# Performance work log

Hardware: AMD Instinct MI355X
Metric: run time of the kernel (lower is better)

The kernel has to match this reference:

```python
import jax, jax.numpy as jnp
import numpy as np

K_SIGN = 100000.0   # tanh sharpness approximating sign()
EPS = 1e-05         # acos clamp epsilon


def setup_inputs() -> dict:
    key = jax.random.key(0)
    B, N, KV = 2, 8, 64
    contour = jax.random.uniform(key, (B, N, KV, 2), dtype=jnp.float32)  # values in [0,1]
    return {"contour": contour, "size": 128}


def reference(contour, size):
    b, n, kv, _ = contour.shape
    dt = contour.dtype
    # pixel grid, normalized by size (matches torch meshgrid 'ij' + reshape(-1,2)/size)
    g = jnp.arange(size, dtype=dt)
    mesh = jnp.stack(jnp.meshgrid(g, g, indexing="ij"), axis=-1).reshape(-1, 2) / size  # (S2, 2)

    c = contour.reshape(b * n, 1, kv, 2)          # (bn, 1, kv, 2)
    diff = c - mesh[None, :, None, :]             # (bn, S2, kv, 2)
    roll_diff = jnp.roll(diff, -1, axis=2)        # next vertex

    # sign = diff * swap(roll_diff); sign[...,1]-sign[...,0] = d_y*rd_x - d_x*rd_y
    cross = diff[..., 1] * roll_diff[..., 0] - diff[..., 0] * roll_diff[..., 1]
    sign = jnp.tanh(K_SIGN * cross)               # (bn, S2, kv)

    norm_diff = jnp.linalg.norm(diff, axis=3)
    norm_roll = jnp.linalg.norm(roll_diff, axis=3)
    scalar = jnp.sum(diff * roll_diff, axis=3)
    cosang = jnp.clip(scalar / (norm_diff * norm_roll), -1.0 + EPS, 1.0 - EPS)
    angles = jnp.arccos(cosang)                   # (bn, S2, kv)

    sum_angles = jnp.clip(jnp.abs(jnp.sum(sign * angles, axis=2) / (2.0 * jnp.pi)), 0.0, 1.0)
    return sum_angles.reshape(b, n, size, size)
```

## Files before the change

### kernel.cpp

```cpp
#include <hip/hip_runtime.h>
#include <math.h>

#define BLOCK 256
#define MAX_KV_LDS 1024


__device__ __forceinline__ float fast_tanh(float t)
{
    float e = __expf(2.0f * t);
    return 1.0f - 2.0f * __builtin_amdgcn_rcpf(e + 1.0f);
}

__device__ __forceinline__ float fast_acos(float x)
{
    float y = fabsf(x);
    float p = -0.0187293f;
    p = fmaf(p, y, 0.0742610f);
    p = fmaf(p, y, -0.2121144f);
    p = fmaf(p, y, 1.5707288f);
    float a = sqrtf(1.0f - y) * p;
    return (x >= 0.0f) ? a : (3.14159265358979f - a);
}

template <typename VP>
__device__ __forceinline__ float winding_sum(VP vsrc, int kv, float mx, float my)
{
    float acc = 0.0f;
    float2 v0 = vsrc[0];
    float dx = v0.x - mx;
    float dy = v0.y - my;
    const float d0x = dx, d0y = dy;
    float nd2 = fmaf(dx, dx, dy * dy);
    const float nd02 = nd2;

    #pragma unroll 4
    for (int k = 0; k < kv - 1; ++k) {
        float2 vn = vsrc[k + 1];
        float rx = vn.x - mx;
        float ry = vn.y - my;
        float cross = dy * rx - dx * ry;
        float dot   = fmaf(dx, rx, dy * ry);
        float nr2   = fmaf(rx, rx, ry * ry);
        float cosang = dot * __builtin_amdgcn_rsqf(nd2 * nr2);
        cosang = fminf(fmaxf(cosang, -1.0f + 1e-5f), 1.0f - 1e-5f);
        acc = fmaf(fast_tanh(100000.0f * cross), fast_acos(cosang), acc);
        dx = rx; dy = ry; nd2 = nr2;
    }
    {
        float cross = dy * d0x - dx * d0y;
        float dot   = fmaf(dx, d0x, dy * d0y);
        float cosang = dot * __builtin_amdgcn_rsqf(nd2 * nd02);
        cosang = fminf(fmaxf(cosang, -1.0f + 1e-5f), 1.0f - 1e-5f);
        acc = fmaf(fast_tanh(100000.0f * cross), fast_acos(cosang), acc);
    }
    return acc;
}

__global__ __launch_bounds__(BLOCK)
void contour_mask_kernel(const float2* __restrict__ contour,
                         const int* __restrict__ size_ptr,
                         float* __restrict__ out,
                         int out_size, int in0_elems)
{
    __shared__ float2 verts[MAX_KV_LDS];

    const int size     = *size_ptr;
    const int S2       = size * size;
    const int bn_total = out_size / S2;
    const int kv       = in0_elems / (bn_total * 2);

    const int idx     = blockIdx.x * BLOCK + threadIdx.x;
    const int bn0     = (blockIdx.x * BLOCK) / S2;
    const int bn_last = (blockIdx.x * BLOCK + BLOCK - 1) / S2;
    const bool use_lds = (kv <= MAX_KV_LDS) && (bn0 == bn_last);

    if (use_lds) {
        for (int i = threadIdx.x; i < kv; i += BLOCK)
            verts[i] = contour[(size_t)bn0 * kv + i];
    }
    __syncthreads();

    if (idx >= out_size) return;

    const int bn = idx / S2;
    const int p  = idx - bn * S2;
    const float inv_size = 1.0f / (float)size;
    const int pi = p / size;
    const int pj = p - pi * size;
    const float mx = (float)pi * inv_size;
    const float my = (float)pj * inv_size;

    float acc;
    if (use_lds)
        acc = winding_sum(verts, kv, mx, my);
    else
        acc = winding_sum(contour + (size_t)bn * kv, kv, mx, my);

    float res = fabsf(acc) * 0.15915494309189535f;
    res = fminf(res, 1.0f);
    out[idx] = res;
}

extern "C" void kernel_launch(void* const* d_in, const int* in_sizes, int n_in,
                              void* d_out, int out_size, void* d_ws, size_t ws_size,
                              hipStream_t stream)
{
    const float2* contour  = (const float2*)d_in[0];
    const int*    size_ptr = (const int*)d_in[1];
    float*        out      = (float*)d_out;

    const int blocks = (out_size + BLOCK - 1) / BLOCK;
    contour_mask_kernel<<<blocks, BLOCK, 0, stream>>>(
        contour, size_ptr, out, out_size, in_sizes[0]);
}
```

Before: 76.60 us.

## Split vertex loop across four lanes per pixel with shuffle reduction

Each pixel's winding sum over the contour vertices is now computed by four adjacent lanes, each covering a quarter of the edges, and combined with xor shuffles. This quadruples the thread count so that a small problem (262k pixels) can better fill the GPU and shorten each thread's serial chain. The clamp is also swapped for fmed3 and the tanh scale is folded into a constant. In exchange there are four times as many blocks, a modulo branch inside the loop, and shuffle overhead, and only one lane in four does the store.

Result: no change. 77.79 us (+1.6%).

```diff
diff --git a/kernel.cpp b/kernel.cpp
--- a/kernel.cpp
+++ b/kernel.cpp
@@ -2,20 +2,19 @@
 #include <math.h>
 
 #define BLOCK 256
+#define SPLIT 4
 #define MAX_KV_LDS 1024
 
-
-__device__ __forceinline__ float fast_tanh(float t)
+__device__ __forceinline__ float fast_tanh_k(float cross)
 {
-    float e = __expf(2.0f * t);
-    return 1.0f - 2.0f * __builtin_amdgcn_rcpf(e + 1.0f);
+    float e = __expf(cross * 200000.0f);
+    return fmaf(-2.0f, __builtin_amdgcn_rcpf(e + 1.0f), 1.0f);
 }
 
 __device__ __forceinline__ float fast_acos(float x)
 {
     float y = fabsf(x);
-    float p = -0.0187293f;
-    p = fmaf(p, y, 0.0742610f);
+    float p = fmaf(-0.0187293f, y, 0.0742610f);
     p = fmaf(p, y, -0.2121144f);
     p = fmaf(p, y, 1.5707288f);
     float a = sqrtf(1.0f - y) * p;
@@ -23,35 +22,28 @@
 }
 
 template <typename VP>
-__device__ __forceinline__ float winding_sum(VP vsrc, int kv, float mx, float my)
+__device__ __forceinline__ float winding_partial(VP vsrc, int kv, int k0, int k1,
+                                                 float mx, float my)
 {
     float acc = 0.0f;
-    float2 v0 = vsrc[0];
-    float dx = v0.x - mx;
-    float dy = v0.y - my;
-    const float d0x = dx, d0y = dy;
+    if (k0 >= k1) return acc;
+    float2 v = vsrc[k0];
+    float dx = v.x - mx, dy = v.y - my;
     float nd2 = fmaf(dx, dx, dy * dy);
-    const float nd02 = nd2;
 
     #pragma unroll 4
-    for (int k = 0; k < kv - 1; ++k) {
-        float2 vn = vsrc[k + 1];
-        float rx = vn.x - mx;
-        float ry = vn.y - my;
+    for (int k = k0; k < k1; ++k) {
+        int kn = k + 1;
+        if (kn == kv) kn = 0;
+        float2 vn = vsrc[kn];
+        float rx = vn.x - mx, ry = vn.y - my;
         float cross = dy * rx - dx * ry;
         float dot   = fmaf(dx, rx, dy * ry);
         float nr2   = fmaf(rx, rx, ry * ry);
         float cosang = dot * __builtin_amdgcn_rsqf(nd2 * nr2);
-        cosang = fminf(fmaxf(cosang, -1.0f + 1e-5f), 1.0f - 1e-5f);
-        acc = fmaf(fast_tanh(100000.0f * cross), fast_acos(cosang), acc);
+        cosang = __builtin_amdgcn_fmed3f(cosang, -1.0f + 1e-5f, 1.0f - 1e-5f);
+        acc = fmaf(fast_tanh_k(cross), fast_acos(cosang), acc);
         dx = rx; dy = ry; nd2 = nr2;
-    }
-    {
-        float cross = dy * d0x - dx * d0y;
-        float dot   = fmaf(dx, d0x, dy * d0y);
-        float cosang = dot * __builtin_amdgcn_rsqf(nd2 * nd02);
-        cosang = fminf(fmaxf(cosang, -1.0f + 1e-5f), 1.0f - 1e-5f);
-        acc = fmaf(fast_tanh(100000.0f * cross), fast_acos(cosang), acc);
     }
     return acc;
 }
@@ -69,36 +61,49 @@
     const int bn_total = out_size / S2;
     const int kv       = in0_elems / (bn_total * 2);
 
-    const int idx     = blockIdx.x * BLOCK + threadIdx.x;
-    const int bn0     = (blockIdx.x * BLOCK) / S2;
-    const int bn_last = (blockIdx.x * BLOCK + BLOCK - 1) / S2;
-    const bool use_lds = (kv <= MAX_KV_LDS) && (bn0 == bn_last);
+    const int tid   = threadIdx.x;
+    const int idx4  = blockIdx.x * BLOCK + tid;
+    const int pixel = idx4 >> 2;
+    const int seg   = tid & (SPLIT - 1);
+
+    const int p_first = (blockIdx.x * BLOCK) >> 2;
+    const int p_last  = ((blockIdx.x + 1) * BLOCK - 1) >> 2;
+    const int bn0     = p_first / S2;
+    const bool use_lds = (kv <= MAX_KV_LDS) && (bn0 == p_last / S2);
 
     if (use_lds) {
-        for (int i = threadIdx.x; i < kv; i += BLOCK)
+        for (int i = tid; i < kv; i += BLOCK)
             verts[i] = contour[(size_t)bn0 * kv + i];
     }
     __syncthreads();
 
-    if (idx >= out_size) return;
+    float acc = 0.0f;
+    if (pixel < out_size) {
+        const int bn = pixel / S2;
+        const int p  = pixel - bn * S2;
+        const float inv_size = 1.0f / (float)size;
+        const int pi = p / size;
+        const int pj = p - pi * size;
+        const float mx = (float)pi * inv_size;
+        const float my = (float)pj * inv_size;
 
-    const int bn = idx / S2;
-    const int p  = idx - bn * S2;
-    const float inv_size = 1.0f / (float)size;
-    const int pi = p / size;
-    const int pj = p - pi * size;
-    const float mx = (float)pi * inv_size;
-    const float my = (float)pj * inv_size;
+        const int q  = (kv + SPLIT - 1) / SPLIT;
+        const int k0 = seg * q;
+        const int k1 = min(k0 + q, kv);
 
-    float acc;
-    if (use_lds)
-        acc = winding_sum(verts, kv, mx, my);
-    else
-        acc = winding_sum(contour + (size_t)bn * kv, kv, mx, my);
+        if (use_lds)
+            acc = winding_partial(verts, kv, k0, k1, mx, my);
+        else
+            acc = winding_partial(contour + (size_t)bn * kv, kv, k0, k1, mx, my);
+    }
 
-    float res = fabsf(acc) * 0.15915494309189535f;
-    res = fminf(res, 1.0f);
-    out[idx] = res;
+    acc += __shfl_xor(acc, 1, 64);
+    acc += __shfl_xor(acc, 2, 64);
+
+    if (pixel < out_size && seg == 0) {
+        float res = fabsf(acc) * 0.15915494309189535f;
+        out[pixel] = fminf(res, 1.0f);
+    }
 }
 
 extern "C" void kernel_launch(void* const* d_in, const int* in_sizes, int n_in,
@@ -109,7 +114,8 @@
     const int*    size_ptr = (const int*)d_in[1];
     float*        out      = (float*)d_out;
 
-    const int blocks = (out_size + BLOCK - 1) / BLOCK;
+    const long long threads = (long long)out_size * SPLIT;
+    const int blocks = (int)((threads + BLOCK - 1) / BLOCK);
     contour_mask_kernel<<<blocks, BLOCK, 0, stream>>>(
         contour, size_ptr, out, out_size, in_sizes[0]);
 }
```
